# Performance work log

Hardware: AMD Instinct MI355X
Metric: run time of the kernel (lower is better)

Reference implementation:

```python
import jax, jax.numpy as jnp
import numpy as np

N = 50000
E = 800000
D_IN, D_HID, D_OUT = 128, 128, 64
BN_EPS = 1e-5

def _glorot(key, shape):
    fan_in = shape[-1]
    return jax.random.normal(key, shape, dtype=jnp.float32) / jnp.sqrt(jnp.float32(fan_in))

def setup_inputs() -> dict:
    key = jax.random.key(0)
    ks = jax.random.split(key, 16)
    x = jax.random.normal(ks[0], (N, D_IN), dtype=jnp.float32)
    edge_index = jax.random.randint(ks[1], (2, E), 0, N, dtype=jnp.int64)
    edge_pairs = jax.random.randint(ks[2], (2, E), 0, N, dtype=jnp.int64)
    return {
        "x": x,
        "edge_index": edge_index,
        "edge_pairs": edge_pairs,
        # SAGEConv1: lin_l (bias) on aggregated neighbors, lin_r (no bias) on root
        "c1_Wl": _glorot(ks[3], (D_HID, D_IN)),
        "c1_bl": jnp.zeros((D_HID,), jnp.float32),
        "c1_Wr": _glorot(ks[4], (D_HID, D_IN)),
        # BatchNorm1d (eval mode: running stats)
        "bn_gamma": jnp.ones((D_HID,), jnp.float32),
        "bn_beta": jnp.zeros((D_HID,), jnp.float32),
        "bn_mean": jnp.zeros((D_HID,), jnp.float32),
        "bn_var": jnp.ones((D_HID,), jnp.float32),
        # SAGEConv2
        "c2_Wl": _glorot(ks[5], (D_OUT, D_HID)),
        "c2_bl": jnp.zeros((D_OUT,), jnp.float32),
        "c2_Wr": _glorot(ks[6], (D_OUT, D_HID)),
        # EdgeRegHead MLP: Linear(2*D_OUT, D_OUT) -> ReLU -> Linear(D_OUT, D_OUT//2) -> ReLU -> Linear(D_OUT//2, 1) -> Sigmoid
        "e_W1": _glorot(ks[7], (D_OUT, 2 * D_OUT)),
        "e_b1": jnp.zeros((D_OUT,), jnp.float32),
        "e_W2": _glorot(ks[8], (D_OUT // 2, D_OUT)),
        "e_b2": jnp.zeros((D_OUT // 2,), jnp.float32),
        "e_W3": _glorot(ks[9], (1, D_OUT // 2)),
        "e_b3": jnp.zeros((1,), jnp.float32),
    }

def _sage_conv(x, src, dst, Wl, bl, Wr):
    # mean-aggregate source features at destination nodes (PyG SAGEConv mean aggr)
    msg_sum = jax.ops.segment_sum(x[src], dst, num_segments=N)          # [N, d]
    cnt = jax.ops.segment_sum(jnp.ones((src.shape[0],), x.dtype), dst, num_segments=N)
    mean = msg_sum / jnp.maximum(cnt, 1.0)[:, None]
    return mean @ Wl.T + bl + x @ Wr.T

def reference(x, edge_index, edge_pairs,
              c1_Wl, c1_bl, c1_Wr,
              bn_gamma, bn_beta, bn_mean, bn_var,
              c2_Wl, c2_bl, c2_Wr,
              e_W1, e_b1, e_W2, e_b2, e_W3, e_b3):
    src, dst = edge_index[0], edge_index[1]
    h = _sage_conv(x, src, dst, c1_Wl, c1_bl, c1_Wr)                    # [N, D_HID]
    h = (h - bn_mean) * jax.lax.rsqrt(bn_var + BN_EPS) * bn_gamma + bn_beta
    h = jax.nn.relu(h)                                                   # dropout inactive (eval)
    z = _sage_conv(h, src, dst, c2_Wl, c2_bl, c2_Wr)                    # [N, D_OUT]
    zi = z[edge_pairs[0]]                                               # [P, D_OUT]
    zj = z[edge_pairs[1]]
    e = jnp.concatenate([zi, zj], axis=-1)                              # [P, 2*D_OUT]
    e = jax.nn.relu(e @ e_W1.T + e_b1)
    e = jax.nn.relu(e @ e_W2.T + e_b2)
    return jax.nn.sigmoid(e @ e_W3.T + e_b3)                            # [P, 1]
```

## Files before the change

kernel.cpp:

```cpp
#include <hip/hip_runtime.h>
#include <hip/hip_bf16.h>
#include <math.h>

#define NN 50000
#define NE 800000
#define DIN 128
#define DHID 128
#define DOUT 64
#define BN_EPS 1e-5f

typedef __attribute__((ext_vector_type(8))) short bf16x8;
typedef __attribute__((ext_vector_type(8))) _Float16 f16x8;
typedef __attribute__((ext_vector_type(4))) _Float16 f16x4;
typedef __attribute__((ext_vector_type(2))) _Float16 f16x2;
typedef __attribute__((ext_vector_type(4))) float f32x4;
typedef unsigned short ushort_t;
typedef unsigned int uint_t;

__device__ __forceinline__ ushort_t f2bf(float f) {
    uint_t u = __float_as_uint(f);
    uint_t r = (u + 0x7FFFu + ((u >> 16) & 1u)) >> 16;
    return (ushort_t)r;
}

__device__ __forceinline__ uint_t pk2bf(float a, float b) {
    __hip_bfloat16 x = __float2bfloat16(a);
    __hip_bfloat16 y = __float2bfloat16(b);
    ushort_t ux = *reinterpret_cast<ushort_t*>(&x);
    ushort_t uy = *reinterpret_cast<ushort_t*>(&y);
    return (uint_t)ux | ((uint_t)uy << 16);
}

__global__ __launch_bounds__(256) void k_deg_xcast(
    const int* __restrict__ ei, int* __restrict__ deg,
    const float* __restrict__ x, _Float16* __restrict__ xh)
{
    int b = blockIdx.x;
    if (b < 3125) {
        int e = b * 256 + threadIdx.x;
        atomicAdd(deg + ei[NE + e], 1);
    } else {
        int i = (b - 3125) * 256 + threadIdx.x;
        const float4* src = (const float4*)x + (size_t)i * 2;
        float4 a = src[0], c = src[1];
        f16x8 o;
        o[0] = (_Float16)a.x; o[1] = (_Float16)a.y; o[2] = (_Float16)a.z; o[3] = (_Float16)a.w;
        o[4] = (_Float16)c.x; o[5] = (_Float16)c.y; o[6] = (_Float16)c.z; o[7] = (_Float16)c.w;
        *(f16x8*)(xh + (size_t)i * 8) = o;
    }
}

__global__ __launch_bounds__(256) void k_scan1_prep(
    const int* __restrict__ deg, int* __restrict__ part,
    const float* __restrict__ c1_Wl, const float* __restrict__ c1_Wr,
    const float* __restrict__ c2_Wl, const float* __restrict__ c2_Wr,
    const float* __restrict__ gam, const float* __restrict__ bet,
    const float* __restrict__ bmean, const float* __restrict__ bvar,
    const float* __restrict__ eW1, const float* __restrict__ eW2,
    _Float16* __restrict__ w1cat, _Float16* __restrict__ w2cat,
    ushort_t* __restrict__ w1bf, ushort_t* __restrict__ w2bf,
    float* __restrict__ bnsc, float* __restrict__ bnsh)
{
    int t = threadIdx.x;
    if (blockIdx.x < 49) {
        __shared__ int s[256];
        int g = blockIdx.x * 256 + t;
        int v = 0;
        if (g < 12500) { int4 d = ((const int4*)deg)[g]; v = d.x + d.y + d.z + d.w; }
        s[t] = v;
        __syncthreads();
        #pragma unroll
        for (int off = 128; off > 0; off >>= 1) {
            if (t < off) s[t] += s[t + off];
            __syncthreads();
        }
        if (t == 0) part[blockIdx.x] = s[0];
    } else {
        for (int i = t; i < 128 * 128; i += 256) {
            int row = i >> 7, k = i & 127;
            w1cat[row * 256 + k]       = (_Float16)c1_Wl[i];
            w1cat[row * 256 + 128 + k] = (_Float16)c1_Wr[i];
        }
        for (int i = t; i < 64 * 128; i += 256) {
            int row = i >> 7, k = i & 127;
            w2cat[row * 256 + k]       = (_Float16)c2_Wl[i];
            w2cat[row * 256 + 128 + k] = (_Float16)c2_Wr[i];
        }
        for (int i = t; i < 64 * 128; i += 256) w1bf[i] = f2bf(eW1[i]);
        for (int i = t; i < 32 * 64; i += 256)  w2bf[i] = f2bf(eW2[i]);
        for (int i = t; i < 128; i += 256) {
            float s = gam[i] * rsqrtf(bvar[i] + BN_EPS);
            bnsc[i] = s;
            bnsh[i] = bet[i] - bmean[i] * s;
        }
    }
}

__global__ __launch_bounds__(256) void k_scan3(
    const int* __restrict__ deg, const int* __restrict__ part, int* __restrict__ rowptr)
{
    __shared__ int s[256];
    __shared__ int p[64];
    int t = threadIdx.x;
    int b = blockIdx.x;
    int g = b * 256 + t;
    int4 d = make_int4(0, 0, 0, 0);
    if (g < 12500) d = ((const int4*)deg)[g];
    int sum4 = d.x + d.y + d.z + d.w;
    s[t] = sum4;
    if (t < 49) p[t] = part[t];
    __syncthreads();
    #pragma unroll
    for (int off = 1; off < 256; off <<= 1) {
        int v = (t >= off) ? s[t - off] : 0;
        __syncthreads();
        s[t] += v;
        __syncthreads();
    }
    int blockoff = 0;
    for (int i = 0; i < b; ++i) blockoff += p[i];
    int off0 = blockoff + s[t] - sum4;
    if (g < 12500) {
        int4 o;
        o.x = off0;
        o.y = off0 + d.x;
        o.z = o.y + d.y;
        o.w = o.z + d.z;
        ((int4*)rowptr)[g] = o;
        if (g == 12499) rowptr[NN] = o.w + d.w;
    }
}

__global__ __launch_bounds__(256) void k_fill(
    const int* __restrict__ ei, const int* __restrict__ rowptr,
    int* __restrict__ cursor, int* __restrict__ csr_src)
{
    int e = blockIdx.x * blockDim.x + threadIdx.x;
    if (e >= NE) return;
    int dst = ei[NE + e];
    int slot = atomicAdd(cursor + dst, 1);
    csr_src[rowptr[dst] + slot] = ei[e];
}

__global__ __launch_bounds__(256) void k_gather_mean_h(
    const _Float16* __restrict__ feat, const int* __restrict__ rowptr,
    const int* __restrict__ csr_src, _Float16* __restrict__ mean)
{
    int wv = (blockIdx.x * blockDim.x + threadIdx.x) >> 6;
    int lane = threadIdx.x & 63;
    if (wv >= NN) return;
    int beg = rowptr[wv], end = rowptr[wv + 1];

    float2 a0 = {0.f, 0.f}, a1 = {0.f, 0.f}, a2 = {0.f, 0.f}, a3 = {0.f, 0.f};
    float2 a4 = {0.f, 0.f}, a5 = {0.f, 0.f}, a6 = {0.f, 0.f}, a7 = {0.f, 0.f};
    int j = beg;
    for (; j + 7 < end; j += 8) {
        int s0 = csr_src[j];
        int s1 = csr_src[j + 1];
        int s2 = csr_src[j + 2];
        int s3 = csr_src[j + 3];
        int s4 = csr_src[j + 4];
        int s5 = csr_src[j + 5];
        int s6 = csr_src[j + 6];
        int s7 = csr_src[j + 7];
        f16x2 v0 = *(const f16x2*)(feat + (size_t)s0 * 128 + lane * 2);
        f16x2 v1 = *(const f16x2*)(feat + (size_t)s1 * 128 + lane * 2);
        f16x2 v2 = *(const f16x2*)(feat + (size_t)s2 * 128 + lane * 2);
        f16x2 v3 = *(const f16x2*)(feat + (size_t)s3 * 128 + lane * 2);
        f16x2 v4 = *(const f16x2*)(feat + (size_t)s4 * 128 + lane * 2);
        f16x2 v5 = *(const f16x2*)(feat + (size_t)s5 * 128 + lane * 2);
        f16x2 v6 = *(const f16x2*)(feat + (size_t)s6 * 128 + lane * 2);
        f16x2 v7 = *(const f16x2*)(feat + (size_t)s7 * 128 + lane * 2);
        a0.x += (float)v0[0]; a0.y += (float)v0[1];
        a1.x += (float)v1[0]; a1.y += (float)v1[1];
        a2.x += (float)v2[0]; a2.y += (float)v2[1];
        a3.x += (float)v3[0]; a3.y += (float)v3[1];
        a4.x += (float)v4[0]; a4.y += (float)v4[1];
        a5.x += (float)v5[0]; a5.y += (float)v5[1];
        a6.x += (float)v6[0]; a6.y += (float)v6[1];
        a7.x += (float)v7[0]; a7.y += (float)v7[1];
    }
    for (; j + 1 < end; j += 2) {
        int s0 = csr_src[j];
        int s1 = csr_src[j + 1];
        f16x2 v0 = *(const f16x2*)(feat + (size_t)s0 * 128 + lane * 2);
        f16x2 v1 = *(const f16x2*)(feat + (size_t)s1 * 128 + lane * 2);
        a0.x += (float)v0[0]; a0.y += (float)v0[1];
        a1.x += (float)v1[0]; a1.y += (float)v1[1];
    }
    if (j < end) {
        int s0 = csr_src[j];
        f16x2 v0 = *(const f16x2*)(feat + (size_t)s0 * 128 + lane * 2);
        a0.x += (float)v0[0]; a0.y += (float)v0[1];
    }
    float inv = 1.0f / fmaxf((float)(end - beg), 1.0f);
    f16x2 o;
    o[0] = (_Float16)((a0.x + a1.x + a2.x + a3.x + a4.x + a5.x + a6.x + a7.x) * inv);
    o[1] = (_Float16)((a0.y + a1.y + a2.y + a3.y + a4.y + a5.y + a6.y + a7.y) * inv);
    *(f16x2*)(mean + (size_t)wv * 128 + lane * 2) = o;
}

__global__ __launch_bounds__(256) void k_conv1_mfma(
    const _Float16* __restrict__ xh, const _Float16* __restrict__ meanh,
    const _Float16* __restrict__ w1cat, const float* __restrict__ bl,
    const float* __restrict__ bnsc, const float* __restrict__ bnsh,
    _Float16* __restrict__ hh)
{
    const int tid = threadIdx.x;
    const int lane = tid & 63;
    const int e = lane & 15;
    const int c = lane >> 4;
    const int chunk = tid >> 6;
    const int tile = blockIdx.x;
    const int node = tile * 16 + e;

    f16x8 wf[2][8];
    #pragma unroll
    for (int nt = 0; nt < 2; ++nt)
        #pragma unroll
        for (int ks = 0; ks < 8; ++ks)
            wf[nt][ks] = *(const f16x8*)(w1cat + (size_t)(chunk * 32 + nt * 16 + e) * 256 + ks * 32 + c * 8);

    f32x4 acc[2];
    #pragma unroll
    for (int nt = 0; nt < 2; ++nt)
        acc[nt] = *(const f32x4*)(bl + chunk * 32 + nt * 16 + c * 4);

    f16x8 bf[8];
    #pragma unroll
    for (int ks = 0; ks < 4; ++ks)
        bf[ks] = *(const f16x8*)(meanh + (size_t)node * 128 + ks * 32 + c * 8);
    #pragma unroll
    for (int ks = 4; ks < 8; ++ks)
        bf[ks] = *(const f16x8*)(xh + (size_t)node * 128 + (ks - 4) * 32 + c * 8);

    #pragma unroll
    for (int ks = 0; ks < 8; ++ks)
        #pragma unroll
        for (int nt = 0; nt < 2; ++nt)
            acc[nt] = __builtin_amdgcn_mfma_f32_16x16x32_f16(wf[nt][ks], bf[ks], acc[nt], 0, 0, 0);

    #pragma unroll
    for (int nt = 0; nt < 2; ++nt) {
        int j0 = chunk * 32 + nt * 16 + c * 4;
        f32x4 sc = *(const f32x4*)(bnsc + j0);
        f32x4 sh = *(const f32x4*)(bnsh + j0);
        f16x4 o;
        #pragma unroll
        for (int r = 0; r < 4; ++r)
            o[r] = (_Float16)fmaxf(acc[nt][r] * sc[r] + sh[r], 0.f);
        *(f16x4*)(hh + (size_t)node * 128 + j0) = o;
    }
}

__global__ __launch_bounds__(256) void k_conv2_mfma(
    const _Float16* __restrict__ hh, const _Float16* __restrict__ meanh,
    const _Float16* __restrict__ w2cat, const float* __restrict__ bl,
    ushort_t* __restrict__ zbf)
{
    const int tid = threadIdx.x;
    const int lane = tid & 63;
    const int e = lane & 15;
    const int c = lane >> 4;
    const int chunk = tid >> 6;
    const int tile = blockIdx.x;
    const int node = tile * 16 + e;

    f16x8 wf[8];
    #pragma unroll
    for (int ks = 0; ks < 8; ++ks)
        wf[ks] = *(const f16x8*)(w2cat + (size_t)(chunk * 16 + e) * 256 + ks * 32 + c * 8);

    f32x4 acc = *(const f32x4*)(bl + chunk * 16 + c * 4);

    f16x8 bf[8];
    #pragma unroll
    for (int ks = 0; ks < 4; ++ks)
        bf[ks] = *(const f16x8*)(meanh + (size_t)node * 128 + ks * 32 + c * 8);
    #pragma unroll
    for (int ks = 4; ks < 8; ++ks)
        bf[ks] = *(const f16x8*)(hh + (size_t)node * 128 + (ks - 4) * 32 + c * 8);

    #pragma unroll
    for (int ks = 0; ks < 8; ++ks)
        acc = __builtin_amdgcn_mfma_f32_16x16x32_f16(wf[ks], bf[ks], acc, 0, 0, 0);

    int j0 = chunk * 16 + c * 4;
    uint2 pk;
    pk.x = pk2bf(acc[0], acc[1]);
    pk.y = pk2bf(acc[2], acc[3]);
    *(uint2*)(zbf + (size_t)node * 64 + j0) = pk;
}

__global__ __launch_bounds__(256) void k_edge(
    const ushort_t* __restrict__ zbf, const int* __restrict__ ep,
    const ushort_t* __restrict__ w1bf, const float* __restrict__ b1,
    const ushort_t* __restrict__ w2bf, const float* __restrict__ b2,
    const float* __restrict__ W3, const float* __restrict__ b3,
    float* __restrict__ out)
{
    __shared__ ushort_t a1lds[4][16 * 64];
    const int tid  = threadIdx.x;
    const int lane = tid & 63;
    const int e    = lane & 15;
    const int c    = lane >> 4;
    ushort_t* lds  = &a1lds[tid >> 6][0];
    const uint_t swz = (uint_t)((e & 7) << 4);

    bf16x8 w1f[4][4];
    #pragma unroll
    for (int mt = 0; mt < 4; ++mt)
        #pragma unroll
        for (int ks = 0; ks < 4; ++ks)
            w1f[mt][ks] = *(const bf16x8*)(w1bf + (mt * 16 + e) * 128 + ks * 32 + c * 8);

    bf16x8 w2f[2][2];
    #pragma unroll
    for (int mt2 = 0; mt2 < 2; ++mt2)
        #pragma unroll
        for (int ks2 = 0; ks2 < 2; ++ks2)
            w2f[mt2][ks2] = *(const bf16x8*)(w2bf + (mt2 * 16 + e) * 64 + ks2 * 32 + c * 8);

    f32x4 bias1[4];
    #pragma unroll
    for (int mt = 0; mt < 4; ++mt) bias1[mt] = *(const f32x4*)(b1 + mt * 16 + c * 4);
    f32x4 bias2[2];
    #pragma unroll
    for (int mt2 = 0; mt2 < 2; ++mt2) bias2[mt2] = *(const f32x4*)(b2 + mt2 * 16 + c * 4);
    f32x4 w3v[2];
    #pragma unroll
    for (int mt2 = 0; mt2 < 2; ++mt2) w3v[mt2] = *(const f32x4*)(W3 + mt2 * 16 + c * 4);
    const float b3v = b3[0];

    const int nw = (gridDim.x * blockDim.x) >> 6;
    const int NT = NE / 16;

#define LOADZ(T, dst)                                                         \
    {                                                                         \
        int p = (T) * 16 + e;                                                 \
        int ni = ep[p];                                                       \
        int nj = ep[NE + p];                                                  \
        const ushort_t* zi = zbf + (size_t)ni * DOUT;                         \
        const ushort_t* zj = zbf + (size_t)nj * DOUT;                         \
        dst[0] = *(const bf16x8*)(zi + c * 8);                                \
        dst[1] = *(const bf16x8*)(zi + 32 + c * 8);                           \
        dst[2] = *(const bf16x8*)(zj + c * 8);                                \
        dst[3] = *(const bf16x8*)(zj + 32 + c * 8);                           \
    }

#define COMPUTE(T, bfr)                                                       \
    {                                                                         \
        f32x4 acc[4];                                                         \
        _Pragma("unroll")                                                     \
        for (int mt = 0; mt < 4; ++mt) acc[mt] = bias1[mt];                   \
        _Pragma("unroll")                                                     \
        for (int ks = 0; ks < 4; ++ks)                                        \
            _Pragma("unroll")                                                 \
            for (int mt = 0; mt < 4; ++mt)                                    \
                acc[mt] = __builtin_amdgcn_mfma_f32_16x16x32_bf16(            \
                    w1f[mt][ks], bfr[ks], acc[mt], 0, 0, 0);                  \
        _Pragma("unroll")                                                     \
        for (int mt = 0; mt < 4; ++mt) {                                      \
            uint_t lo = pk2bf(fmaxf(acc[mt][0], 0.f), fmaxf(acc[mt][1], 0.f));\
            uint_t hi = pk2bf(fmaxf(acc[mt][2], 0.f), fmaxf(acc[mt][3], 0.f));\
            uint_t off = (uint_t)(e * 128 + mt * 32 + c * 8) ^ swz;           \
            *(uint2*)((char*)lds + off) = make_uint2(lo, hi);                 \
        }                                                                     \
        bf16x8 b2f[2];                                                        \
        _Pragma("unroll")                                                     \
        for (int ks2 = 0; ks2 < 2; ++ks2) {                                   \
            uint_t off = (uint_t)(e * 128 + ks2 * 64 + c * 16) ^ swz;         \
            b2f[ks2] = *(const bf16x8*)((const char*)lds + off);              \
        }                                                                     \
        f32x4 a2[2];                                                          \
        _Pragma("unroll")                                                     \
        for (int mt2 = 0; mt2 < 2; ++mt2) a2[mt2] = bias2[mt2];               \
        _Pragma("unroll")                                                     \
        for (int ks2 = 0; ks2 < 2; ++ks2)                                     \
            _Pragma("unroll")                                                 \
            for (int mt2 = 0; mt2 < 2; ++mt2)                                 \
                a2[mt2] = __builtin_amdgcn_mfma_f32_16x16x32_bf16(            \
                    w2f[mt2][ks2], b2f[ks2], a2[mt2], 0, 0, 0);               \
        float t3 = b3v;                                                       \
        _Pragma("unroll")                                                     \
        for (int mt2 = 0; mt2 < 2; ++mt2)                                     \
            _Pragma("unroll")                                                 \
            for (int r = 0; r < 4; ++r)                                       \
                t3 += fmaxf(a2[mt2][r], 0.f) * w3v[mt2][r];                   \
        t3 += __shfl_xor(t3, 16);                                             \
        t3 += __shfl_xor(t3, 32);                                             \
        if (lane < 16) {                                                      \
            float ex = __expf(-t3);                                           \
            out[(T) * 16 + lane] = __builtin_amdgcn_rcpf(1.f + ex);           \
        }                                                                     \
    }

    bf16x8 zA[4], zB[4];
    int tile = (blockIdx.x * blockDim.x + tid) >> 6;
    if (tile >= NT) return;
    LOADZ(tile, zA);
    while (tile < NT) {
        int nx = tile + nw;
        if (nx < NT) LOADZ(nx, zB);
        COMPUTE(tile, zA);
        tile = nx;
        if (tile >= NT) break;
        nx = tile + nw;
        if (nx < NT) LOADZ(nx, zA);
        COMPUTE(tile, zB);
        tile = nx;
    }

#undef LOADZ
#undef COMPUTE
}

extern "C" void kernel_launch(void* const* d_in, const int* in_sizes, int n_in,
                              void* d_out, int out_size, void* d_ws, size_t ws_size,
                              hipStream_t stream)
{
    const float* x     = (const float*)d_in[0];
    const int*   ei    = (const int*)d_in[1];
    const int*   ep    = (const int*)d_in[2];
    const float* c1_Wl = (const float*)d_in[3];
    const float* c1_bl = (const float*)d_in[4];
    const float* c1_Wr = (const float*)d_in[5];
    const float* bn_g  = (const float*)d_in[6];
    const float* bn_b  = (const float*)d_in[7];
    const float* bn_m  = (const float*)d_in[8];
    const float* bn_v  = (const float*)d_in[9];
    const float* c2_Wl = (const float*)d_in[10];
    const float* c2_bl = (const float*)d_in[11];
    const float* c2_Wr = (const float*)d_in[12];
    const float* e_W1  = (const float*)d_in[13];
    const float* e_b1  = (const float*)d_in[14];
    const float* e_W2  = (const float*)d_in[15];
    const float* e_b2  = (const float*)d_in[16];
    const float* e_W3  = (const float*)d_in[17];
    const float* e_b3  = (const float*)d_in[18];
    float* out = (float*)d_out;

    _Float16* xh    = (_Float16*)d_ws;
    _Float16* meanh = xh + (size_t)NN * DIN;
    _Float16* hh    = meanh + (size_t)NN * DIN;
    ushort_t* zbf   = (ushort_t*)(hh + (size_t)NN * DHID);
    _Float16* w1cat = (_Float16*)(zbf + (size_t)NN * DOUT);
    _Float16* w2cat = w1cat + 128 * 256;
    ushort_t* w1bf  = (ushort_t*)(w2cat + 64 * 256);
    ushort_t* w2bf  = w1bf + 64 * 128;
    float*    bnsc  = (float*)(w2bf + 32 * 64);
    float*    bnsh  = bnsc + 128;
    int*      deg     = (int*)(bnsh + 128);
    int*      cursor  = deg + 50048;
    int*      rowptr  = cursor + 50048;
    int*      csr_src = rowptr + 50052;
    int*      part    = csr_src + 800000;

    hipMemsetAsync(deg, 0, (size_t)(50048 * 2) * sizeof(int), stream);

    k_deg_xcast<<<6250, 256, 0, stream>>>(ei, deg, x, xh);
    k_scan1_prep<<<50, 256, 0, stream>>>(deg, part,
                                         c1_Wl, c1_Wr, c2_Wl, c2_Wr,
                                         bn_g, bn_b, bn_m, bn_v, e_W1, e_W2,
                                         w1cat, w2cat, w1bf, w2bf, bnsc, bnsh);
    k_scan3<<<49, 256, 0, stream>>>(deg, part, rowptr);
    k_fill <<<3125, 256, 0, stream>>>(ei, rowptr, cursor, csr_src);

    k_gather_mean_h<<<12500, 256, 0, stream>>>(xh, rowptr, csr_src, meanh);
    k_conv1_mfma<<<3125, 256, 0, stream>>>(xh, meanh, w1cat, c1_bl, bnsc, bnsh, hh);

    k_gather_mean_h<<<12500, 256, 0, stream>>>(hh, rowptr, csr_src, meanh);
    k_conv2_mfma<<<3125, 256, 0, stream>>>(hh, meanh, w2cat, c2_bl, zbf);

    k_edge<<<1024, 256, 0, stream>>>(zbf, ep, w1bf, e_b1, w2bf, e_b2,
                                     e_W3, e_b3, out);
}
```

Before: 303.0 us.

## Fuse neighbor mean gather into SAGE conv MFMA kernels via LDS

Merges the separate gather-mean kernels into the conv1 and conv2 MFMA kernels. Each block gathers the neighbor means for its 16 nodes into swizzled LDS, then feeds them straight to the MFMAs. This removes the meanh round trip through global memory and two kernel launches. In exchange, each wave now handles 4 nodes serially during the gather, which lowers gather parallelism. The change also adds s_setprio around the MFMA sections in the edge kernel and raises the edge grid from 1024 to 1280 blocks.

```diff
diff --git a/kernel.cpp b/kernel.cpp
--- a/kernel.cpp
+++ b/kernel.cpp
@@ -142,76 +142,75 @@
     csr_src[rowptr[dst] + slot] = ei[e];
 }
 
-__global__ __launch_bounds__(256) void k_gather_mean_h(
-    const _Float16* __restrict__ feat, const int* __restrict__ rowptr,
-    const int* __restrict__ csr_src, _Float16* __restrict__ mean)
-{
-    int wv = (blockIdx.x * blockDim.x + threadIdx.x) >> 6;
-    int lane = threadIdx.x & 63;
-    if (wv >= NN) return;
-    int beg = rowptr[wv], end = rowptr[wv + 1];
-
-    float2 a0 = {0.f, 0.f}, a1 = {0.f, 0.f}, a2 = {0.f, 0.f}, a3 = {0.f, 0.f};
-    float2 a4 = {0.f, 0.f}, a5 = {0.f, 0.f}, a6 = {0.f, 0.f}, a7 = {0.f, 0.f};
-    int j = beg;
-    for (; j + 7 < end; j += 8) {
-        int s0 = csr_src[j];
-        int s1 = csr_src[j + 1];
-        int s2 = csr_src[j + 2];
-        int s3 = csr_src[j + 3];
-        int s4 = csr_src[j + 4];
-        int s5 = csr_src[j + 5];
-        int s6 = csr_src[j + 6];
-        int s7 = csr_src[j + 7];
-        f16x2 v0 = *(const f16x2*)(feat + (size_t)s0 * 128 + lane * 2);
-        f16x2 v1 = *(const f16x2*)(feat + (size_t)s1 * 128 + lane * 2);
-        f16x2 v2 = *(const f16x2*)(feat + (size_t)s2 * 128 + lane * 2);
-        f16x2 v3 = *(const f16x2*)(feat + (size_t)s3 * 128 + lane * 2);
-        f16x2 v4 = *(const f16x2*)(feat + (size_t)s4 * 128 + lane * 2);
-        f16x2 v5 = *(const f16x2*)(feat + (size_t)s5 * 128 + lane * 2);
-        f16x2 v6 = *(const f16x2*)(feat + (size_t)s6 * 128 + lane * 2);
-        f16x2 v7 = *(const f16x2*)(feat + (size_t)s7 * 128 + lane * 2);
-        a0.x += (float)v0[0]; a0.y += (float)v0[1];
-        a1.x += (float)v1[0]; a1.y += (float)v1[1];
-        a2.x += (float)v2[0]; a2.y += (float)v2[1];
-        a3.x += (float)v3[0]; a3.y += (float)v3[1];
-        a4.x += (float)v4[0]; a4.y += (float)v4[1];
-        a5.x += (float)v5[0]; a5.y += (float)v5[1];
-        a6.x += (float)v6[0]; a6.y += (float)v6[1];
-        a7.x += (float)v7[0]; a7.y += (float)v7[1];
-    }
-    for (; j + 1 < end; j += 2) {
-        int s0 = csr_src[j];
-        int s1 = csr_src[j + 1];
-        f16x2 v0 = *(const f16x2*)(feat + (size_t)s0 * 128 + lane * 2);
-        f16x2 v1 = *(const f16x2*)(feat + (size_t)s1 * 128 + lane * 2);
-        a0.x += (float)v0[0]; a0.y += (float)v0[1];
-        a1.x += (float)v1[0]; a1.y += (float)v1[1];
-    }
-    if (j < end) {
-        int s0 = csr_src[j];
-        f16x2 v0 = *(const f16x2*)(feat + (size_t)s0 * 128 + lane * 2);
-        a0.x += (float)v0[0]; a0.y += (float)v0[1];
-    }
-    float inv = 1.0f / fmaxf((float)(end - beg), 1.0f);
-    f16x2 o;
-    o[0] = (_Float16)((a0.x + a1.x + a2.x + a3.x + a4.x + a5.x + a6.x + a7.x) * inv);
-    o[1] = (_Float16)((a0.y + a1.y + a2.y + a3.y + a4.y + a5.y + a6.y + a7.y) * inv);
-    *(f16x2*)(mean + (size_t)wv * 128 + lane * 2) = o;
-}
-
-__global__ __launch_bounds__(256) void k_conv1_mfma(
-    const _Float16* __restrict__ xh, const _Float16* __restrict__ meanh,
+#define GATHER4(feat)                                                          \
+    {                                                                          \
+        _Pragma("unroll 1")                                                    \
+        for (int q = 0; q < 4; ++q) {                                          \
+            int n = w * 4 + q;                                                 \
+            int node = tile * 16 + n;                                          \
+            int beg = __builtin_amdgcn_readfirstlane(rowptr[node]);            \
+            int end = __builtin_amdgcn_readfirstlane(rowptr[node + 1]);        \
+            float2 a0 = {0.f,0.f}, a1 = {0.f,0.f}, a2 = {0.f,0.f}, a3 = {0.f,0.f}; \
+            float2 a4 = {0.f,0.f}, a5 = {0.f,0.f}, a6 = {0.f,0.f}, a7 = {0.f,0.f}; \
+            int j = beg;                                                       \
+            for (; j + 7 < end; j += 8) {                                      \
+                int s0 = csr_src[j];     int s1 = csr_src[j + 1];              \
+                int s2 = csr_src[j + 2]; int s3 = csr_src[j + 3];              \
+                int s4 = csr_src[j + 4]; int s5 = csr_src[j + 5];              \
+                int s6 = csr_src[j + 6]; int s7 = csr_src[j + 7];              \
+                f16x2 v0 = *(const f16x2*)(feat + (size_t)s0 * 128 + lane * 2);\
+                f16x2 v1 = *(const f16x2*)(feat + (size_t)s1 * 128 + lane * 2);\
+                f16x2 v2 = *(const f16x2*)(feat + (size_t)s2 * 128 + lane * 2);\
+                f16x2 v3 = *(const f16x2*)(feat + (size_t)s3 * 128 + lane * 2);\
+                f16x2 v4 = *(const f16x2*)(feat + (size_t)s4 * 128 + lane * 2);\
+                f16x2 v5 = *(const f16x2*)(feat + (size_t)s5 * 128 + lane * 2);\
+                f16x2 v6 = *(const f16x2*)(feat + (size_t)s6 * 128 + lane * 2);\
+                f16x2 v7 = *(const f16x2*)(feat + (size_t)s7 * 128 + lane * 2);\
+                a0.x += (float)v0[0]; a0.y += (float)v0[1];                    \
+                a1.x += (float)v1[0]; a1.y += (float)v1[1];                    \
+                a2.x += (float)v2[0]; a2.y += (float)v2[1];                    \
+                a3.x += (float)v3[0]; a3.y += (float)v3[1];                    \
+                a4.x += (float)v4[0]; a4.y += (float)v4[1];                    \
+                a5.x += (float)v5[0]; a5.y += (float)v5[1];                    \
+                a6.x += (float)v6[0]; a6.y += (float)v6[1];                    \
+                a7.x += (float)v7[0]; a7.y += (float)v7[1];                    \
+            }                                                                  \
+            for (; j + 1 < end; j += 2) {                                      \
+                int s0 = csr_src[j];                                           \
+                int s1 = csr_src[j + 1];                                       \
+                f16x2 v0 = *(const f16x2*)(feat + (size_t)s0 * 128 + lane * 2);\
+                f16x2 v1 = *(const f16x2*)(feat + (size_t)s1 * 128 + lane * 2);\
+                a0.x += (float)v0[0]; a0.y += (float)v0[1];                    \
+                a1.x += (float)v1[0]; a1.y += (float)v1[1];                    \
+            }                                                                  \
+            if (j < end) {                                                     \
+                int s0 = csr_src[j];                                           \
+                f16x2 v0 = *(const f16x2*)(feat + (size_t)s0 * 128 + lane * 2);\
+                a0.x += (float)v0[0]; a0.y += (float)v0[1];                    \
+            }                                                                  \
+            float inv = 1.0f / fmaxf((float)(end - beg), 1.0f);                \
+            f16x2 o;                                                           \
+            o[0] = (_Float16)((a0.x + a1.x + a2.x + a3.x + a4.x + a5.x + a6.x + a7.x) * inv); \
+            o[1] = (_Float16)((a0.y + a1.y + a2.y + a3.y + a4.y + a5.y + a6.y + a7.y) * inv); \
+            uint_t off = (uint_t)(n * 256 + lane * 4) ^ (uint_t)((n & 7) << 4);\
+            *(f16x2*)((char*)mlds + off) = o;                                  \
+        }                                                                      \
+    }
+
+__global__ __launch_bounds__(256) void k_gconv1(
+    const _Float16* __restrict__ xh, const int* __restrict__ rowptr,
+    const int* __restrict__ csr_src,
     const _Float16* __restrict__ w1cat, const float* __restrict__ bl,
     const float* __restrict__ bnsc, const float* __restrict__ bnsh,
     _Float16* __restrict__ hh)
 {
+    __shared__ _Float16 mlds[16 * 128];
     const int tid = threadIdx.x;
     const int lane = tid & 63;
+    const int w = tid >> 6;
+    const int tile = blockIdx.x;
     const int e = lane & 15;
     const int c = lane >> 4;
-    const int chunk = tid >> 6;
-    const int tile = blockIdx.x;
     const int node = tile * 16 + e;
 
     f16x8 wf[2][8];
@@ -219,30 +218,40 @@
     for (int nt = 0; nt < 2; ++nt)
         #pragma unroll
         for (int ks = 0; ks < 8; ++ks)
-            wf[nt][ks] = *(const f16x8*)(w1cat + (size_t)(chunk * 32 + nt * 16 + e) * 256 + ks * 32 + c * 8);
-
+            wf[nt][ks] = *(const f16x8*)(w1cat + (size_t)(w * 32 + nt * 16 + e) * 256 + ks * 32 + c * 8);
+    f16x8 bfx[4];
+    #pragma unroll
+    for (int ks = 0; ks < 4; ++ks)
+        bfx[ks] = *(const f16x8*)(xh + (size_t)node * 128 + ks * 32 + c * 8);
     f32x4 acc[2];
     #pragma unroll
     for (int nt = 0; nt < 2; ++nt)
-        acc[nt] = *(const f32x4*)(bl + chunk * 32 + nt * 16 + c * 4);
-
-    f16x8 bf[8];
-    #pragma unroll
-    for (int ks = 0; ks < 4; ++ks)
-        bf[ks] = *(const f16x8*)(meanh + (size_t)node * 128 + ks * 32 + c * 8);
-    #pragma unroll
-    for (int ks = 4; ks < 8; ++ks)
-        bf[ks] = *(const f16x8*)(xh + (size_t)node * 128 + (ks - 4) * 32 + c * 8);
-
-    #pragma unroll
-    for (int ks = 0; ks < 8; ++ks)
+        acc[nt] = *(const f32x4*)(bl + w * 32 + nt * 16 + c * 4);
+
+    GATHER4(xh);
+    __syncthreads();
+
+    f16x8 bfm[4];
+    #pragma unroll
+    for (int ks = 0; ks < 4; ++ks) {
+        uint_t off = (uint_t)(e * 256 + ks * 64 + c * 16) ^ (uint_t)((e & 7) << 4);
+        bfm[ks] = *(const f16x8*)((const char*)mlds + off);
+    }
+
+    #pragma unroll
+    for (int ks = 0; ks < 4; ++ks)
         #pragma unroll
         for (int nt = 0; nt < 2; ++nt)
-            acc[nt] = __builtin_amdgcn_mfma_f32_16x16x32_f16(wf[nt][ks], bf[ks], acc[nt], 0, 0, 0);
+            acc[nt] = __builtin_amdgcn_mfma_f32_16x16x32_f16(wf[nt][ks], bfm[ks], acc[nt], 0, 0, 0);
+    #pragma unroll
+    for (int ks = 0; ks < 4; ++ks)
+        #pragma unroll
+        for (int nt = 0; nt < 2; ++nt)
+            acc[nt] = __builtin_amdgcn_mfma_f32_16x16x32_f16(wf[nt][ks + 4], bfx[ks], acc[nt], 0, 0, 0);
 
     #pragma unroll
     for (int nt = 0; nt < 2; ++nt) {
-        int j0 = chunk * 32 + nt * 16 + c * 4;
+        int j0 = w * 32 + nt * 16 + c * 4;
         f32x4 sc = *(const f32x4*)(bnsc + j0);
         f32x4 sh = *(const f32x4*)(bnsh + j0);
         f16x4 o;
@@ -253,39 +262,49 @@
     }
 }
 
-__global__ __launch_bounds__(256) void k_conv2_mfma(
-    const _Float16* __restrict__ hh, const _Float16* __restrict__ meanh,
+__global__ __launch_bounds__(256) void k_gconv2(
+    const _Float16* __restrict__ hh, const int* __restrict__ rowptr,
+    const int* __restrict__ csr_src,
     const _Float16* __restrict__ w2cat, const float* __restrict__ bl,
     ushort_t* __restrict__ zbf)
 {
+    __shared__ _Float16 mlds[16 * 128];
     const int tid = threadIdx.x;
     const int lane = tid & 63;
+    const int w = tid >> 6;
+    const int tile = blockIdx.x;
     const int e = lane & 15;
     const int c = lane >> 4;
-    const int chunk = tid >> 6;
-    const int tile = blockIdx.x;
     const int node = tile * 16 + e;
 
     f16x8 wf[8];
     #pragma unroll
     for (int ks = 0; ks < 8; ++ks)
-        wf[ks] = *(const f16x8*)(w2cat + (size_t)(chunk * 16 + e) * 256 + ks * 32 + c * 8);
-
-    f32x4 acc = *(const f32x4*)(bl + chunk * 16 + c * 4);
-
-    f16x8 bf[8];
-    #pragma unroll
-    for (int ks = 0; ks < 4; ++ks)
-        bf[ks] = *(const f16x8*)(meanh + (size_t)node * 128 + ks * 32 + c * 8);
-    #pragma unroll
-    for (int ks = 4; ks < 8; ++ks)
-        bf[ks] = *(const f16x8*)(hh + (size_t)node * 128 + (ks - 4) * 32 + c * 8);
-
-    #pragma unroll
-    for (int ks = 0; ks < 8; ++ks)
-        acc = __builtin_amdgcn_mfma_f32_16x16x32_f16(wf[ks], bf[ks], acc, 0, 0, 0);
-
-    int j0 = chunk * 16 + c * 4;
+        wf[ks] = *(const f16x8*)(w2cat + (size_t)(w * 16 + e) * 256 + ks * 32 + c * 8);
+    f16x8 bfx[4];
+    #pragma unroll
+    for (int ks = 0; ks < 4; ++ks)
+        bfx[ks] = *(const f16x8*)(hh + (size_t)node * 128 + ks * 32 + c * 8);
+    f32x4 acc = *(const f32x4*)(bl + w * 16 + c * 4);
+
+    GATHER4(hh);
+    __syncthreads();
+
+    f16x8 bfm[4];
+    #pragma unroll
+    for (int ks = 0; ks < 4; ++ks) {
+        uint_t off = (uint_t)(e * 256 + ks * 64 + c * 16) ^ (uint_t)((e & 7) << 4);
+        bfm[ks] = *(const f16x8*)((const char*)mlds + off);
+    }
+
+    #pragma unroll
+    for (int ks = 0; ks < 4; ++ks)
+        acc = __builtin_amdgcn_mfma_f32_16x16x32_f16(wf[ks], bfm[ks], acc, 0, 0, 0);
+    #pragma unroll
+    for (int ks = 0; ks < 4; ++ks)
+        acc = __builtin_amdgcn_mfma_f32_16x16x32_f16(wf[ks + 4], bfx[ks], acc, 0, 0, 0);
+
+    int j0 = w * 16 + c * 4;
     uint2 pk;
     pk.x = pk2bf(acc[0], acc[1]);
     pk.y = pk2bf(acc[2], acc[3]);
@@ -353,12 +372,14 @@
         f32x4 acc[4];                                                         \
         _Pragma("unroll")                                                     \
         for (int mt = 0; mt < 4; ++mt) acc[mt] = bias1[mt];                   \
+        __builtin_amdgcn_s_setprio(1);                                        \
         _Pragma("unroll")                                                     \
         for (int ks = 0; ks < 4; ++ks)                                        \
             _Pragma("unroll")                                                 \
             for (int mt = 0; mt < 4; ++mt)                                    \
                 acc[mt] = __builtin_amdgcn_mfma_f32_16x16x32_bf16(            \
                     w1f[mt][ks], bfr[ks], acc[mt], 0, 0, 0);                  \
+        __builtin_amdgcn_s_setprio(0);                                        \
         _Pragma("unroll")                                                     \
         for (int mt = 0; mt < 4; ++mt) {                                      \
             uint_t lo = pk2bf(fmaxf(acc[mt][0], 0.f), fmaxf(acc[mt][1], 0.f));\
@@ -375,12 +396,14 @@
         f32x4 a2[2];                                                          \
         _Pragma("unroll")                                                     \
         for (int mt2 = 0; mt2 < 2; ++mt2) a2[mt2] = bias2[mt2];               \
+        __builtin_amdgcn_s_setprio(1);                                        \
         _Pragma("unroll")                                                     \
         for (int ks2 = 0; ks2 < 2; ++ks2)                                     \
             _Pragma("unroll")                                                 \
             for (int mt2 = 0; mt2 < 2; ++mt2)                                 \
                 a2[mt2] = __builtin_amdgcn_mfma_f32_16x16x32_bf16(            \
                     w2f[mt2][ks2], b2f[ks2], a2[mt2], 0, 0, 0);               \
+        __builtin_amdgcn_s_setprio(0);                                        \
         float t3 = b3v;                                                       \
         _Pragma("unroll")                                                     \
         for (int mt2 = 0; mt2 < 2; ++mt2)                                     \
@@ -466,12 +489,9 @@
     k_scan3<<<49, 256, 0, stream>>>(deg, part, rowptr);
     k_fill <<<3125, 256, 0, stream>>>(ei, rowptr, cursor, csr_src);
 
-    k_gather_mean_h<<<12500, 256, 0, stream>>>(xh, rowptr, csr_src, meanh);
-    k_conv1_mfma<<<3125, 256, 0, stream>>>(xh, meanh, w1cat, c1_bl, bnsc, bnsh, hh);
-
-    k_gather_mean_h<<<12500, 256, 0, stream>>>(hh, rowptr, csr_src, meanh);
-    k_conv2_mfma<<<3125, 256, 0, stream>>>(hh, meanh, w2cat, c2_bl, zbf);
-
-    k_edge<<<1024, 256, 0, stream>>>(zbf, ep, w1bf, e_b1, w2bf, e_b2,
+    k_gconv1<<<3125, 256, 0, stream>>>(xh, rowptr, csr_src, w1cat, c1_bl, bnsc, bnsh, hh);
+    k_gconv2<<<3125, 256, 0, stream>>>(hh, rowptr, csr_src, w2cat, c2_bl, zbf);
+
+    k_edge<<<1280, 256, 0, stream>>>(zbf, ep, w1bf, e_b1, w2bf, e_b2,
                                      e_W3, e_b3, out);
 }
```

Result: faster. 295.7 us (-2.4%).
